# Optimization experiments

Measured on AMD Instinct MI355X. Metric: run time of the kernel, lower is better.

The kernel has to match this reference:

```python
import jax, jax.numpy as jnp
import numpy as np

EPS = 1e-6
B, L = 4, 2048


def _quat_normalize(q):
    # unit-normalize quaternions along last dim
    return q / (jnp.linalg.norm(q, axis=-1, keepdims=True) + 1e-12)


def setup_inputs() -> dict:
    key = jax.random.key(0)
    k1, k2 = jax.random.split(key)
    genomic_quats = jax.random.normal(k1, (B, L, 4), dtype=jnp.float32)
    code_quats = jax.random.normal(k2, (B, L, 4), dtype=jnp.float32)
    return {"genomic_quats": genomic_quats, "code_quats": code_quats}


def reference(genomic_quats, code_quats):
    # normalize to SU(2) and take imaginary (i,j,k) parts as R^3 paths
    path_a = _quat_normalize(genomic_quats)[..., 1:]  # [B, L, 3]
    path_b = _quat_normalize(code_quats)[..., 1:]

    # segment tangents and midpoints
    dr_a = path_a[:, 1:, :] - path_a[:, :-1, :]          # [B, L-1, 3]
    dr_b = path_b[:, 1:, :] - path_b[:, :-1, :]
    r_a = (path_a[:, 1:, :] + path_a[:, :-1, :]) * 0.5
    r_b = (path_b[:, 1:, :] + path_b[:, :-1, :]) * 0.5

    # all-pairs Gauss linking kernel
    r_diff = r_a[:, :, None, :] - r_b[:, None, :, :]     # [B, L-1, L-1, 3]
    dist = jnp.linalg.norm(r_diff, axis=-1) + EPS        # [B, L-1, L-1]
    cross = jnp.cross(dr_a[:, :, None, :], dr_b[:, None, :, :], axis=-1)
    numerator = jnp.sum(r_diff * cross, axis=-1)         # triple product
    kernel = numerator / dist ** 3
    linking = jnp.sum(kernel, axis=(1, 2)) / (4.0 * jnp.pi)  # [B]
    return jnp.mean(jnp.abs(linking))
```

## Files before the change

### kernel.cpp

```cpp
#include <hip/hip_runtime.h>
#include <math.h>

#define LQ 2048
#define NB 4
#define NSEG 2047
#define MI 4
#define JC 8
#define PARTIALS_PER_B 512

__device__ __forceinline__ float rcp_fast(float x)  { return __builtin_amdgcn_rcpf(x); }
__device__ __forceinline__ float rsq_fast(float x)  { return __builtin_amdgcn_rsqf(x); }

__device__ __forceinline__ void make_seg(float4 q0, float4 q1,
                                         float dr[3], float r[3], float m[3]) {
    float n2a = fmaf(q0.x, q0.x, fmaf(q0.y, q0.y, fmaf(q0.z, q0.z, q0.w * q0.w)));
    float s0  = rsq_fast(n2a);
    float ax = q0.y * s0, ay = q0.z * s0, az = q0.w * s0;
    float n2b = fmaf(q1.x, q1.x, fmaf(q1.y, q1.y, fmaf(q1.z, q1.z, q1.w * q1.w)));
    float s1  = rsq_fast(n2b);
    float bx = q1.y * s1, by = q1.z * s1, bz = q1.w * s1;
    dr[0] = bx - ax; dr[1] = by - ay; dr[2] = bz - az;
    r[0] = 0.5f * (ax + bx); r[1] = 0.5f * (ay + by); r[2] = 0.5f * (az + bz);
    m[0] = r[1] * dr[2] - r[2] * dr[1];
    m[1] = r[2] * dr[0] - r[0] * dr[2];
    m[2] = r[0] * dr[1] - r[1] * dr[0];
}

__global__ __launch_bounds__(256) void pair_fused(const float4* __restrict__ qa,
                                                  const float4* __restrict__ qb,
                                                  float* __restrict__ partials) {
    const int jc    = blockIdx.x;
    const int itile = blockIdx.y;
    const int b     = blockIdx.z;
    const int t     = threadIdx.x;

    __shared__ float js[JC][12];
    if (t < JC) {
        int j = jc * JC + t;
        float dr[3] = {0.f, 0.f, 0.f}, r[3] = {0.f, 0.f, 0.f}, m[3] = {0.f, 0.f, 0.f};
        if (j < NSEG) {
            float4 q0 = qb[b * LQ + j];
            float4 q1 = qb[b * LQ + j + 1];
            make_seg(q0, q1, dr, r, m);
        }
        js[t][0] = dr[0]; js[t][1] = dr[1]; js[t][2] = dr[2];
        js[t][3] = r[0];  js[t][4] = r[1];  js[t][5] = r[2];
        js[t][6] = m[0];  js[t][7] = m[1];  js[t][8] = m[2];
        js[t][9] = 0.f;   js[t][10] = 0.f;  js[t][11] = 0.f;
    }

    float dra[MI][3], ra[MI][3], ma[MI][3];
#pragma unroll
    for (int k = 0; k < MI; k++) {
        int i = itile * 1024 + k * 256 + t;
        if (i < NSEG) {
            float4 q0 = qa[b * LQ + i];
            float4 q1 = qa[b * LQ + i + 1];
            make_seg(q0, q1, dra[k], ra[k], ma[k]);
        } else {
#pragma unroll
            for (int c = 0; c < 3; c++) { dra[k][c] = 0.f; ra[k][c] = 0.f; ma[k][c] = 0.f; }
        }
    }

    __syncthreads();

    float acc = 0.0f;
#pragma unroll
    for (int jj = 0; jj < JC; jj++) {
        float drbx = js[jj][0], drby = js[jj][1], drbz = js[jj][2];
        float rbx  = js[jj][3], rby  = js[jj][4], rbz  = js[jj][5];
        float mbx  = js[jj][6], mby  = js[jj][7], mbz  = js[jj][8];
#pragma unroll
        for (int k = 0; k < MI; k++) {
            float dx = ra[k][0] - rbx;
            float dy = ra[k][1] - rby;
            float dz = ra[k][2] - rbz;
            float d2 = fmaf(dx, dx, fmaf(dy, dy, fmaf(dz, dz, 1e-12f)));
            float rs = rsq_fast(d2);
            float inv3 = rs * rs * rs;
            float num = fmaf(ma[k][0], drbx,
                        fmaf(ma[k][1], drby,
                        fmaf(ma[k][2], drbz,
                        fmaf(dra[k][0], mbx,
                        fmaf(dra[k][1], mby, dra[k][2] * mbz)))));
            acc = fmaf(num, inv3, acc);
        }
    }

#pragma unroll
    for (int off = 32; off > 0; off >>= 1) acc += __shfl_down(acc, off, 64);
    __shared__ float wsum[4];
    int lane = t & 63, w = t >> 6;
    if (lane == 0) wsum[w] = acc;
    __syncthreads();
    if (t == 0) {
        partials[b * PARTIALS_PER_B + itile * 256 + jc] =
            wsum[0] + wsum[1] + wsum[2] + wsum[3];
    }
}

__global__ __launch_bounds__(256) void finalize_kernel(const float* __restrict__ partials,
                                                       float* __restrict__ out) {
    int t = threadIdx.x;
    int w = t >> 6, lane = t & 63;
    float s = 0.0f;
#pragma unroll
    for (int r = 0; r < PARTIALS_PER_B / 64; r++)
        s += partials[w * PARTIALS_PER_B + r * 64 + lane];
#pragma unroll
    for (int off = 32; off > 0; off >>= 1) s += __shfl_down(s, off, 64);
    __shared__ float sb[4];
    if (lane == 0) sb[w] = s;
    __syncthreads();
    if (t == 0) {
        float tot = fabsf(sb[0]) + fabsf(sb[1]) + fabsf(sb[2]) + fabsf(sb[3]);
        out[0] = tot * (1.0f / NB) * (1.0f / (4.0f * 3.14159265358979323846f));
    }
}

extern "C" void kernel_launch(void* const* d_in, const int* in_sizes, int n_in,
                              void* d_out, int out_size, void* d_ws, size_t ws_size,
                              hipStream_t stream) {
    const float4* qa = (const float4*)d_in[0];
    const float4* qb = (const float4*)d_in[1];
    float* partials = (float*)d_ws;
    float* out = (float*)d_out;

    pair_fused<<<dim3(256, 2, NB), dim3(256), 0, stream>>>(qa, qb, partials);
    finalize_kernel<<<dim3(1), dim3(256), 0, stream>>>(partials, out);
}
```

Before: 66.34 us.

## Fuse finalize into pair kernel via cooperative grid sync, widen j-chunk

Merges the two-kernel launch into one cooperative kernel that writes per-block partials, synchronizes the whole grid, and has block 0 do the final reduction. This removes the second launch and its launch gap. The j-chunk per block doubles to 16, so the grid halves to 1024 blocks, and the shared-memory reads of j data become float4 vector loads. In exchange, a grid-wide barrier is added, and the cooperative launch requires all blocks to be co-resident, which adds its own sync cost.

```diff
diff --git a/kernel.cpp b/kernel.cpp
--- a/kernel.cpp
+++ b/kernel.cpp
@@ -1,15 +1,19 @@
 #include <hip/hip_runtime.h>
+#include <hip/hip_cooperative_groups.h>
 #include <math.h>
+
+namespace cg = cooperative_groups;
 
 #define LQ 2048
 #define NB 4
 #define NSEG 2047
 #define MI 4
-#define JC 8
-#define PARTIALS_PER_B 512
+#define JC 16
+#define NJC 128
+#define NITILE 2
+#define NPART (NB * NITILE * NJC)
 
-__device__ __forceinline__ float rcp_fast(float x)  { return __builtin_amdgcn_rcpf(x); }
-__device__ __forceinline__ float rsq_fast(float x)  { return __builtin_amdgcn_rsqf(x); }
+__device__ __forceinline__ float rsq_fast(float x) { return __builtin_amdgcn_rsqf(x); }
 
 __device__ __forceinline__ void make_seg(float4 q0, float4 q1,
                                          float dr[3], float r[3], float m[3]) {
@@ -26,22 +30,21 @@
     m[2] = r[0] * dr[1] - r[1] * dr[0];
 }
 
-__global__ __launch_bounds__(256) void pair_fused(const float4* __restrict__ qa,
-                                                  const float4* __restrict__ qb,
-                                                  float* __restrict__ partials) {
+__global__ __launch_bounds__(256, 4) void gauss_coop(const float4* __restrict__ qa,
+                                                     const float4* __restrict__ qb,
+                                                     float* __restrict__ partials,
+                                                     float* __restrict__ out) {
     const int jc    = blockIdx.x;
     const int itile = blockIdx.y;
     const int b     = blockIdx.z;
     const int t     = threadIdx.x;
 
-    __shared__ float js[JC][12];
+    __shared__ __align__(16) float js[JC][12];
     if (t < JC) {
         int j = jc * JC + t;
-        float dr[3] = {0.f, 0.f, 0.f}, r[3] = {0.f, 0.f, 0.f}, m[3] = {0.f, 0.f, 0.f};
+        float dr[3] = {0.f,0.f,0.f}, r[3] = {0.f,0.f,0.f}, m[3] = {0.f,0.f,0.f};
         if (j < NSEG) {
-            float4 q0 = qb[b * LQ + j];
-            float4 q1 = qb[b * LQ + j + 1];
-            make_seg(q0, q1, dr, r, m);
+            make_seg(qb[b * LQ + j], qb[b * LQ + j + 1], dr, r, m);
         }
         js[t][0] = dr[0]; js[t][1] = dr[1]; js[t][2] = dr[2];
         js[t][3] = r[0];  js[t][4] = r[1];  js[t][5] = r[2];
@@ -54,9 +57,7 @@
     for (int k = 0; k < MI; k++) {
         int i = itile * 1024 + k * 256 + t;
         if (i < NSEG) {
-            float4 q0 = qa[b * LQ + i];
-            float4 q1 = qa[b * LQ + i + 1];
-            make_seg(q0, q1, dra[k], ra[k], ma[k]);
+            make_seg(qa[b * LQ + i], qa[b * LQ + i + 1], dra[k], ra[k], ma[k]);
         } else {
 #pragma unroll
             for (int c = 0; c < 3; c++) { dra[k][c] = 0.f; ra[k][c] = 0.f; ma[k][c] = 0.f; }
@@ -68,9 +69,11 @@
     float acc = 0.0f;
 #pragma unroll
     for (int jj = 0; jj < JC; jj++) {
-        float drbx = js[jj][0], drby = js[jj][1], drbz = js[jj][2];
-        float rbx  = js[jj][3], rby  = js[jj][4], rbz  = js[jj][5];
-        float mbx  = js[jj][6], mby  = js[jj][7], mbz  = js[jj][8];
+        const float4* r4 = (const float4*)&js[jj][0];
+        float4 A = r4[0], B = r4[1], C = r4[2];
+        float drbx = A.x, drby = A.y, drbz = A.z;
+        float rbx  = A.w, rby  = B.x, rbz  = B.y;
+        float mbx  = B.z, mby  = B.w, mbz  = C.x;
 #pragma unroll
         for (int k = 0; k < MI; k++) {
             float dx = ra[k][0] - rbx;
@@ -78,7 +81,7 @@
             float dz = ra[k][2] - rbz;
             float d2 = fmaf(dx, dx, fmaf(dy, dy, fmaf(dz, dz, 1e-12f)));
             float rs = rsq_fast(d2);
-            float inv3 = rs * rs * rs;
+            float inv3 = (rs * rs) * rs;
             float num = fmaf(ma[k][0], drbx,
                         fmaf(ma[k][1], drby,
                         fmaf(ma[k][2], drbz,
@@ -91,31 +94,29 @@
 #pragma unroll
     for (int off = 32; off > 0; off >>= 1) acc += __shfl_down(acc, off, 64);
     __shared__ float wsum[4];
+    __shared__ float sb[4];
     int lane = t & 63, w = t >> 6;
     if (lane == 0) wsum[w] = acc;
     __syncthreads();
     if (t == 0) {
-        partials[b * PARTIALS_PER_B + itile * 256 + jc] =
+        partials[(b * NITILE + itile) * NJC + jc] =
             wsum[0] + wsum[1] + wsum[2] + wsum[3];
     }
-}
+    __threadfence();
 
-__global__ __launch_bounds__(256) void finalize_kernel(const float* __restrict__ partials,
-                                                       float* __restrict__ out) {
-    int t = threadIdx.x;
-    int w = t >> 6, lane = t & 63;
-    float s = 0.0f;
+    cg::this_grid().sync();
+
+    if (blockIdx.x == 0 && blockIdx.y == 0 && blockIdx.z == 0) {
+        const float* pb = partials + w * (NITILE * NJC);
+        float s = pb[lane] + pb[64 + lane] + pb[128 + lane] + pb[192 + lane];
 #pragma unroll
-    for (int r = 0; r < PARTIALS_PER_B / 64; r++)
-        s += partials[w * PARTIALS_PER_B + r * 64 + lane];
-#pragma unroll
-    for (int off = 32; off > 0; off >>= 1) s += __shfl_down(s, off, 64);
-    __shared__ float sb[4];
-    if (lane == 0) sb[w] = s;
-    __syncthreads();
-    if (t == 0) {
-        float tot = fabsf(sb[0]) + fabsf(sb[1]) + fabsf(sb[2]) + fabsf(sb[3]);
-        out[0] = tot * (1.0f / NB) * (1.0f / (4.0f * 3.14159265358979323846f));
+        for (int off = 32; off > 0; off >>= 1) s += __shfl_down(s, off, 64);
+        if (lane == 0) sb[w] = fabsf(s);
+        __syncthreads();
+        if (t == 0) {
+            out[0] = (sb[0] + sb[1] + sb[2] + sb[3]) *
+                     (1.0f / NB) * (1.0f / (4.0f * 3.14159265358979323846f));
+        }
     }
 }
 
@@ -127,6 +128,8 @@
     float* partials = (float*)d_ws;
     float* out = (float*)d_out;
 
-    pair_fused<<<dim3(256, 2, NB), dim3(256), 0, stream>>>(qa, qb, partials);
-    finalize_kernel<<<dim3(1), dim3(256), 0, stream>>>(partials, out);
+    void* args[] = {(void*)&qa, (void*)&qb, (void*)&partials, (void*)&out};
+    hipLaunchCooperativeKernel((void*)gauss_coop,
+                               dim3(NJC, NITILE, NB), dim3(256),
+                               args, 0, stream);
 }
```

New measurement: 166.7 us. +151.3%, slower.
